# Performance work log

Measured on AMD Instinct MI355X. Metric: run time of the kernel, lower is better.

Reference implementation:

```python
import jax, jax.numpy as jnp
import numpy as np
import math

B, S, D_IN, D_K = 4, 4096, 3, 5

def setup_inputs() -> dict:
    key = jax.random.key(0)
    ks = jax.random.split(key, 7)
    return {
        "x1": jax.random.normal(ks[0], (B, S, D_IN), dtype=jnp.float32),
        "Wq": jax.random.normal(ks[1], (D_K, D_IN), dtype=jnp.float32) / math.sqrt(D_IN),
        "bq": jax.random.normal(ks[2], (D_K,), dtype=jnp.float32) * 0.02,
        "Wk": jax.random.normal(ks[3], (D_K, D_IN), dtype=jnp.float32) / math.sqrt(D_IN),
        "bk": jax.random.normal(ks[4], (D_K,), dtype=jnp.float32) * 0.02,
        "Wv": jax.random.normal(ks[5], (D_K, D_IN), dtype=jnp.float32) / math.sqrt(D_IN),
        "bv": jax.random.normal(ks[6], (D_K,), dtype=jnp.float32) * 0.02,
    }

def reference(x1, Wq, bq, Wk, bk, Wv, bv):
    # q/k/v projections: Linear(d_in -> d_k), weight stored torch-style [out, in]
    q = jnp.einsum('bsd,kd->bsk', x1, Wq) + bq  # [B,S,Dk]
    k = jnp.einsum('bsd,kd->bsk', x1, Wk) + bk
    v = jnp.einsum('bsd,kd->bsk', x1, Wv) + bv
    scale = 1.0 / math.sqrt(q.shape[-1])
    qk = jnp.einsum('bqk,bsk->bqs', q, k) * scale  # [B,S,S]
    # Non-standard: causal mask applied AFTER softmax (elementwise multiply)
    mask = jnp.tril(jnp.ones((q.shape[1], q.shape[1]), dtype=qk.dtype))
    attn = jax.nn.softmax(qk, axis=-1) * mask
    return jnp.einsum('bqs,bsk->bqk', attn, v)  # [B,S,Dk]
```

## Files before the change

### kernel.cpp

```cpp
#include <hip/hip_runtime.h>
#include <math.h>

#define BB 4
#define SS 4096
#define DK 5
#define TK 2048
#define NT 256
#define LAM (0.44721359549995793f * 1.4426950408889634f)

typedef float v2f __attribute__((ext_vector_type(2)));

__device__ __forceinline__ float fast_exp2(float x) {
#if __has_builtin(__builtin_amdgcn_exp2f)
    return __builtin_amdgcn_exp2f(x);
#else
    float r; asm("v_exp_f32 %0, %1" : "=v"(r) : "v"(x)); return r;
#endif
}

__device__ __forceinline__ v2f pk_fma(v2f a, v2f b, v2f c) {
    return __builtin_elementwise_fma(a, b, c);
}

#define GLOAD16(gp, lp)                                                        \
    __builtin_amdgcn_global_load_lds(                                          \
        (const __attribute__((address_space(1))) unsigned int*)(gp),           \
        (__attribute__((address_space(3))) unsigned int*)(lp), 16, 0, 0)

__global__ __launch_bounds__(NT) void proj_x(
    const float* __restrict__ x, float* __restrict__ Xt)
{
    int gid = blockIdx.x * NT + threadIdx.x;
    if (gid >= BB * SS) return;
    int b = gid >> 12;
    int s = gid & (SS - 1);
    float* XtB = Xt + (size_t)b * 3 * SS;
    XtB[0 * SS + s] = x[gid * 3 + 0];
    XtB[1 * SS + s] = x[gid * 3 + 1];
    XtB[2 * SS + s] = x[gid * 3 + 2];
}

__global__ __launch_bounds__(NT, 4) void attn(
    const float* __restrict__ x,
    const float* __restrict__ Wq, const float* __restrict__ bq,
    const float* __restrict__ Wk,
    const float* __restrict__ Wv, const float* __restrict__ bv,
    const float* __restrict__ Xt,
    float* __restrict__ out)
{
    __shared__ float kls[3][TK];

    const int tid = threadIdx.x;
    const int sub = tid & 63;
    const int wave = tid >> 6;

    const int b = blockIdx.x >> 8;
    const int i = blockIdx.x & 255;
    const int lowRow  = i * 8;
    const int highRow = (511 - i) * 8;
    const int row0w = (wave < 2) ? (lowRow + wave * 4) : (highRow + (wave - 2) * 4);

    float M00=0,M01=0,M02=0,M10=0,M11=0,M12=0,M20=0,M21=0,M22=0;
    float u0=0,u1=0,u2=0;
#pragma unroll
    for (int d = 0; d < DK; ++d) {
        float q0 = Wq[d*3+0], q1 = Wq[d*3+1], q2 = Wq[d*3+2];
        float k0 = Wk[d*3+0], k1 = Wk[d*3+1], k2 = Wk[d*3+2];
        float bqd = bq[d];
        M00 = fmaf(q0,k0,M00); M01 = fmaf(q0,k1,M01); M02 = fmaf(q0,k2,M02);
        M10 = fmaf(q1,k0,M10); M11 = fmaf(q1,k1,M11); M12 = fmaf(q1,k2,M12);
        M20 = fmaf(q2,k0,M20); M21 = fmaf(q2,k1,M21); M22 = fmaf(q2,k2,M22);
        u0 = fmaf(k0,bqd,u0);  u1 = fmaf(k1,bqd,u1);  u2 = fmaf(k2,bqd,u2);
    }

    v2f a2[4][3];
#pragma unroll
    for (int r = 0; r < 4; ++r) {
        const float* xr = &x[((size_t)b * SS + row0w + r) * 3];
        float x0 = xr[0], x1 = xr[1], x2 = xr[2];
        float av0 = LAM * (x0*M00 + x1*M10 + x2*M20 + u0);
        float av1 = LAM * (x0*M01 + x1*M11 + x2*M21 + u1);
        float av2 = LAM * (x0*M02 + x1*M12 + x2*M22 + u2);
        a2[r][0] = (v2f){av0, av0};
        a2[r][1] = (v2f){av1, av1};
        a2[r][2] = (v2f){av2, av2};
    }

    float wv0 = 0.f, wv1 = 0.f, wv2 = 0.f, bvl = 0.f;
    if (sub < DK) {
        wv0 = Wv[sub*3+0]; wv1 = Wv[sub*3+1]; wv2 = Wv[sub*3+2]; bvl = bv[sub];
    }

    v2f l2[4];
    v2f acc2[4][4];
#pragma unroll
    for (int r = 0; r < 4; ++r) {
        l2[r] = (v2f){0.f, 0.f};
#pragma unroll
        for (int d = 0; d < 4; ++d) acc2[r][d] = (v2f){0.f, 0.f};
    }

    const float* XtB = Xt + (size_t)b * 3 * SS;

    for (int t = 0; t < SS; t += TK) {
        __syncthreads();
#pragma unroll
        for (int it = 0; it < 6; ++it) {
            int idx = it * NT + tid;
            int d = idx >> 9, c4 = idx & 511;
            GLOAD16(&XtB[(size_t)d * SS + t + c4 * 4], &kls[d][c4 * 4]);
        }
        __syncthreads();

#pragma unroll
        for (int j = 0; j < TK / 256; ++j) {
            const int key = j * 256 + sub * 4;
            const int cstart = t + j * 256;
            const int cend   = cstart + 255;
            const int kbase  = cstart + sub * 4;

            float4 kt0 = *(const float4*)&kls[0][key];
            float4 kt1 = *(const float4*)&kls[1][key];
            float4 kt2 = *(const float4*)&kls[2][key];

            if (cend <= row0w) {
#pragma unroll
                for (int h = 0; h < 2; ++h) {
                    v2f k0 = ((v2f*)&kt0)[h];
                    v2f k1 = ((v2f*)&kt1)[h];
                    v2f k2 = ((v2f*)&kt2)[h];
#pragma unroll
                    for (int r = 0; r < 4; ++r) {
                        v2f sc = pk_fma(a2[r][0], k0,
                                 pk_fma(a2[r][1], k1, a2[r][2] * k2));
                        v2f p;
                        p.x = fast_exp2(sc.x); p.y = fast_exp2(sc.y);
                        l2[r] += p;
                        acc2[r][0] = pk_fma(p, k0, acc2[r][0]);
                        acc2[r][1] = pk_fma(p, k1, acc2[r][1]);
                        acc2[r][2] = pk_fma(p, k2, acc2[r][2]);
                        acc2[r][3] += p;
                    }
                }
            } else if (cstart > row0w + 3) {
#pragma unroll
                for (int h = 0; h < 2; ++h) {
                    v2f k0 = ((v2f*)&kt0)[h];
                    v2f k1 = ((v2f*)&kt1)[h];
                    v2f k2 = ((v2f*)&kt2)[h];
#pragma unroll
                    for (int r = 0; r < 4; ++r) {
                        v2f sc = pk_fma(a2[r][0], k0,
                                 pk_fma(a2[r][1], k1, a2[r][2] * k2));
                        v2f p;
                        p.x = fast_exp2(sc.x); p.y = fast_exp2(sc.y);
                        l2[r] += p;
                    }
                }
            } else {
#pragma unroll
                for (int h = 0; h < 2; ++h) {
                    const int kgh = kbase + h * 2;
                    v2f k0 = ((v2f*)&kt0)[h];
                    v2f k1 = ((v2f*)&kt1)[h];
                    v2f k2 = ((v2f*)&kt2)[h];
#pragma unroll
                    for (int r = 0; r < 4; ++r) {
                        const int row = row0w + r;
                        v2f sc = pk_fma(a2[r][0], k0,
                                 pk_fma(a2[r][1], k1, a2[r][2] * k2));
                        v2f p;
                        p.x = fast_exp2(sc.x); p.y = fast_exp2(sc.y);
                        l2[r] += p;
                        v2f pm;
                        pm.x = (kgh + 0 <= row) ? p.x : 0.f;
                        pm.y = (kgh + 1 <= row) ? p.y : 0.f;
                        acc2[r][0] = pk_fma(pm, k0, acc2[r][0]);
                        acc2[r][1] = pk_fma(pm, k1, acc2[r][1]);
                        acc2[r][2] = pk_fma(pm, k2, acc2[r][2]);
                        acc2[r][3] += pm;
                    }
                }
            }
        }
    }

#pragma unroll
    for (int r = 0; r < 4; ++r) {
        float lr = l2[r].x + l2[r].y;
        float A0 = acc2[r][0].x + acc2[r][0].y;
        float A1 = acc2[r][1].x + acc2[r][1].y;
        float A2 = acc2[r][2].x + acc2[r][2].y;
        float PS = acc2[r][3].x + acc2[r][3].y;
#pragma unroll
        for (int off = 32; off >= 1; off >>= 1) {
            lr += __shfl_xor(lr, off);
            A0 += __shfl_xor(A0, off);
            A1 += __shfl_xor(A1, off);
            A2 += __shfl_xor(A2, off);
            PS += __shfl_xor(PS, off);
        }
        if (sub < DK) {
            float num = fmaf(wv0, A0, fmaf(wv1, A1, fmaf(wv2, A2, bvl * PS)));
            out[((size_t)b * SS + row0w + r) * DK + sub] = num / lr;
        }
    }
}

extern "C" void kernel_launch(void* const* d_in, const int* in_sizes, int n_in,
                              void* d_out, int out_size, void* d_ws, size_t ws_size,
                              hipStream_t stream) {
    const float* x  = (const float*)d_in[0];
    const float* Wq = (const float*)d_in[1];
    const float* bq = (const float*)d_in[2];
    const float* Wk = (const float*)d_in[3];
    const float* Wv = (const float*)d_in[5];
    const float* bv = (const float*)d_in[6];
    float* outp = (float*)d_out;

    float* Xt = (float*)d_ws;

    proj_x<<<(BB * SS + NT - 1) / NT, NT, 0, stream>>>(x, Xt);
    attn<<<BB * (SS / 16), NT, 0, stream>>>(x, Wq, bq, Wk, Wv, bv, Xt, outp);
}
```

Before: 28.44 us.

## Drop transpose kernel and LDS staging; stream keys from global with register double-buffering

Removes the separate transpose pre-kernel and the LDS tile, so each lane reads its four interleaved keys straight from the original x layout with three float4 loads. The next chunk is prefetched into registers while the current one is computed. Each wave now takes two low rows and two high rows instead of four consecutive rows, which evens out causal work within a wave. This saves one launch and the block barriers, but the causal branch is now chosen per row inside the inner loop, which may cause divergence or extra code, and the launch-bounds occupancy hint is gone.

```diff
diff --git a/kernel.cpp b/kernel.cpp
--- a/kernel.cpp
+++ b/kernel.cpp
@@ -4,7 +4,6 @@
 #define BB 4
 #define SS 4096
 #define DK 5
-#define TK 2048
 #define NT 256
 #define LAM (0.44721359549995793f * 1.4426950408889634f)
 
@@ -22,43 +21,22 @@
     return __builtin_elementwise_fma(a, b, c);
 }
 
-#define GLOAD16(gp, lp)                                                        \
-    __builtin_amdgcn_global_load_lds(                                          \
-        (const __attribute__((address_space(1))) unsigned int*)(gp),           \
-        (__attribute__((address_space(3))) unsigned int*)(lp), 16, 0, 0)
-
-__global__ __launch_bounds__(NT) void proj_x(
-    const float* __restrict__ x, float* __restrict__ Xt)
-{
-    int gid = blockIdx.x * NT + threadIdx.x;
-    if (gid >= BB * SS) return;
-    int b = gid >> 12;
-    int s = gid & (SS - 1);
-    float* XtB = Xt + (size_t)b * 3 * SS;
-    XtB[0 * SS + s] = x[gid * 3 + 0];
-    XtB[1 * SS + s] = x[gid * 3 + 1];
-    XtB[2 * SS + s] = x[gid * 3 + 2];
-}
-
-__global__ __launch_bounds__(NT, 4) void attn(
+__global__ __launch_bounds__(NT) void attn(
     const float* __restrict__ x,
     const float* __restrict__ Wq, const float* __restrict__ bq,
     const float* __restrict__ Wk,
     const float* __restrict__ Wv, const float* __restrict__ bv,
-    const float* __restrict__ Xt,
     float* __restrict__ out)
 {
-    __shared__ float kls[3][TK];
-
     const int tid = threadIdx.x;
     const int sub = tid & 63;
     const int wave = tid >> 6;
 
     const int b = blockIdx.x >> 8;
     const int i = blockIdx.x & 255;
-    const int lowRow  = i * 8;
-    const int highRow = (511 - i) * 8;
-    const int row0w = (wave < 2) ? (lowRow + wave * 4) : (highRow + (wave - 2) * 4);
+    const int lo0 = i * 8 + wave * 2;
+    const int hi0 = (511 - i) * 8 + wave * 2;
+    const int rows[4] = {lo0, lo0 + 1, hi0, hi0 + 1};
 
     float M00=0,M01=0,M02=0,M10=0,M11=0,M12=0,M20=0,M21=0,M22=0;
     float u0=0,u1=0,u2=0;
@@ -73,10 +51,12 @@
         u0 = fmaf(k0,bqd,u0);  u1 = fmaf(k1,bqd,u1);  u2 = fmaf(k2,bqd,u2);
     }
 
+    const float* xb = x + (size_t)b * SS * 3;
+
     v2f a2[4][3];
 #pragma unroll
     for (int r = 0; r < 4; ++r) {
-        const float* xr = &x[((size_t)b * SS + row0w + r) * 3];
+        const float* xr = &xb[(size_t)rows[r] * 3];
         float x0 = xr[0], x1 = xr[1], x2 = xr[2];
         float av0 = LAM * (x0*M00 + x1*M10 + x2*M20 + u0);
         float av1 = LAM * (x0*M01 + x1*M11 + x2*M21 + u1);
@@ -100,86 +80,58 @@
         for (int d = 0; d < 4; ++d) acc2[r][d] = (v2f){0.f, 0.f};
     }
 
-    const float* XtB = Xt + (size_t)b * 3 * SS;
-
-    for (int t = 0; t < SS; t += TK) {
-        __syncthreads();
-#pragma unroll
-        for (int it = 0; it < 6; ++it) {
-            int idx = it * NT + tid;
-            int d = idx >> 9, c4 = idx & 511;
-            GLOAD16(&XtB[(size_t)d * SS + t + c4 * 4], &kls[d][c4 * 4]);
-        }
-        __syncthreads();
+    float4 bufA[2], bufB[2], bufC[2];
+    {
+        const float4* p = (const float4*)(xb + (size_t)(sub * 4) * 3);
+        bufA[0] = p[0]; bufB[0] = p[1]; bufC[0] = p[2];
+    }
 
 #pragma unroll
-        for (int j = 0; j < TK / 256; ++j) {
-            const int key = j * 256 + sub * 4;
-            const int cstart = t + j * 256;
-            const int cend   = cstart + 255;
-            const int kbase  = cstart + sub * 4;
+    for (int c = 0; c < SS / 256; ++c) {
+        const int cur = c & 1;
+        if (c < SS / 256 - 1) {
+            const float4* p = (const float4*)(xb + (size_t)((c + 1) * 256 + sub * 4) * 3);
+            bufA[cur ^ 1] = p[0]; bufB[cur ^ 1] = p[1]; bufC[cur ^ 1] = p[2];
+        }
+        const float4 A = bufA[cur], B = bufB[cur], C = bufC[cur];
+        const int cstart = c * 256;
+        const int cend   = cstart + 255;
+        const int kbase  = cstart + sub * 4;
 
-            float4 kt0 = *(const float4*)&kls[0][key];
-            float4 kt1 = *(const float4*)&kls[1][key];
-            float4 kt2 = *(const float4*)&kls[2][key];
-
-            if (cend <= row0w) {
 #pragma unroll
-                for (int h = 0; h < 2; ++h) {
-                    v2f k0 = ((v2f*)&kt0)[h];
-                    v2f k1 = ((v2f*)&kt1)[h];
-                    v2f k2 = ((v2f*)&kt2)[h];
+        for (int h = 0; h < 2; ++h) {
+            const int kgh = kbase + h * 2;
+            v2f k0, k1, k2;
+            if (h == 0) {
+                k0 = (v2f){A.x, A.w};
+                k1 = (v2f){A.y, B.x};
+                k2 = (v2f){A.z, B.y};
+            } else {
+                k0 = (v2f){B.z, C.y};
+                k1 = (v2f){B.w, C.z};
+                k2 = (v2f){C.x, C.w};
+            }
 #pragma unroll
-                    for (int r = 0; r < 4; ++r) {
-                        v2f sc = pk_fma(a2[r][0], k0,
-                                 pk_fma(a2[r][1], k1, a2[r][2] * k2));
-                        v2f p;
-                        p.x = fast_exp2(sc.x); p.y = fast_exp2(sc.y);
-                        l2[r] += p;
-                        acc2[r][0] = pk_fma(p, k0, acc2[r][0]);
-                        acc2[r][1] = pk_fma(p, k1, acc2[r][1]);
-                        acc2[r][2] = pk_fma(p, k2, acc2[r][2]);
-                        acc2[r][3] += p;
-                    }
-                }
-            } else if (cstart > row0w + 3) {
-#pragma unroll
-                for (int h = 0; h < 2; ++h) {
-                    v2f k0 = ((v2f*)&kt0)[h];
-                    v2f k1 = ((v2f*)&kt1)[h];
-                    v2f k2 = ((v2f*)&kt2)[h];
-#pragma unroll
-                    for (int r = 0; r < 4; ++r) {
-                        v2f sc = pk_fma(a2[r][0], k0,
-                                 pk_fma(a2[r][1], k1, a2[r][2] * k2));
-                        v2f p;
-                        p.x = fast_exp2(sc.x); p.y = fast_exp2(sc.y);
-                        l2[r] += p;
-                    }
-                }
-            } else {
-#pragma unroll
-                for (int h = 0; h < 2; ++h) {
-                    const int kgh = kbase + h * 2;
-                    v2f k0 = ((v2f*)&kt0)[h];
-                    v2f k1 = ((v2f*)&kt1)[h];
-                    v2f k2 = ((v2f*)&kt2)[h];
-#pragma unroll
-                    for (int r = 0; r < 4; ++r) {
-                        const int row = row0w + r;
-                        v2f sc = pk_fma(a2[r][0], k0,
-                                 pk_fma(a2[r][1], k1, a2[r][2] * k2));
-                        v2f p;
-                        p.x = fast_exp2(sc.x); p.y = fast_exp2(sc.y);
-                        l2[r] += p;
-                        v2f pm;
-                        pm.x = (kgh + 0 <= row) ? p.x : 0.f;
-                        pm.y = (kgh + 1 <= row) ? p.y : 0.f;
-                        acc2[r][0] = pk_fma(pm, k0, acc2[r][0]);
-                        acc2[r][1] = pk_fma(pm, k1, acc2[r][1]);
-                        acc2[r][2] = pk_fma(pm, k2, acc2[r][2]);
-                        acc2[r][3] += pm;
-                    }
+            for (int r = 0; r < 4; ++r) {
+                const int row = rows[r];
+                v2f sc = pk_fma(a2[r][0], k0,
+                         pk_fma(a2[r][1], k1, a2[r][2] * k2));
+                v2f p;
+                p.x = fast_exp2(sc.x); p.y = fast_exp2(sc.y);
+                l2[r] += p;
+                if (cend <= row) {
+                    acc2[r][0] = pk_fma(p, k0, acc2[r][0]);
+                    acc2[r][1] = pk_fma(p, k1, acc2[r][1]);
+                    acc2[r][2] = pk_fma(p, k2, acc2[r][2]);
+                    acc2[r][3] += p;
+                } else if (cstart <= row) {
+                    v2f pm;
+                    pm.x = (kgh + 0 <= row) ? p.x : 0.f;
+                    pm.y = (kgh + 1 <= row) ? p.y : 0.f;
+                    acc2[r][0] = pk_fma(pm, k0, acc2[r][0]);
+                    acc2[r][1] = pk_fma(pm, k1, acc2[r][1]);
+                    acc2[r][2] = pk_fma(pm, k2, acc2[r][2]);
+                    acc2[r][3] += pm;
                 }
             }
         }
@@ -202,7 +154,7 @@
         }
         if (sub < DK) {
             float num = fmaf(wv0, A0, fmaf(wv1, A1, fmaf(wv2, A2, bvl * PS)));
-            out[((size_t)b * SS + row0w + r) * DK + sub] = num / lr;
+            out[((size_t)b * SS + rows[r]) * DK + sub] = num / lr;
         }
     }
 }
@@ -218,8 +170,5 @@
     const float* bv = (const float*)d_in[6];
     float* outp = (float*)d_out;
 
-    float* Xt = (float*)d_ws;
-
-    proj_x<<<(BB * SS + NT - 1) / NT, NT, 0, stream>>>(x, Xt);
-    attn<<<BB * (SS / 16), NT, 0, stream>>>(x, Wq, bq, Wk, Wv, bv, Xt, outp);
+    attn<<<BB * (SS / 16), NT, 0, stream>>>(x, Wq, bq, Wk, Wv, bv, outp);
 }
```

After: 39.61 us. 39.3% more time.
